# Kernel optimization log

Hardware: AMD Instinct MI355X
Metric: run time of the kernel (lower is better)

## Reference

```python
import jax, jax.numpy as jnp
import numpy as np

DIM = 1024

def _circ_conv(x, key):
    # circular convolution along last dim via FFT
    D = x.shape[-1]
    return jnp.fft.irfft(jnp.fft.rfft(x, axis=-1) * jnp.fft.rfft(key), n=D, axis=-1)

def _circ_corr(x, key):
    # circular correlation: conjugate the key spectrum
    D = x.shape[-1]
    return jnp.fft.irfft(jnp.fft.rfft(x, axis=-1) * jnp.conj(jnp.fft.rfft(key)), n=D, axis=-1)

def setup_inputs() -> dict:
    key = jax.random.key(0)
    k0, k1, k2 = jax.random.split(key, 3)
    B, T, D = 4, 2048, DIM
    x = jax.random.normal(k0, (B, T, D), dtype=jnp.float32)
    bind_key = jax.random.normal(k1, (D,), dtype=jnp.float32) * 0.02
    unbind_key = jax.random.normal(k2, (D,), dtype=jnp.float32) * 0.02
    gate = jnp.ones((1,), dtype=jnp.float32)
    decay = jnp.asarray(0.9, dtype=jnp.float32)
    return {"x": x, "bind_key": bind_key, "unbind_key": unbind_key, "gate": gate, "decay": decay}

def reference(x, bind_key, unbind_key, gate, decay):
    B, T, D = x.shape
    bound = _circ_conv(x, bind_key)                      # (B, T, D)
    d = jax.nn.sigmoid(decay)
    pos = jnp.arange(T, dtype=x.dtype)
    diff = pos[:, None] - pos[None, :]                   # (T, T)
    causal = diff >= 0
    # clamp exponent to avoid inf*0 on masked (t < s) entries; math identical to tril mask
    decay_matrix = jnp.where(causal, d ** jnp.maximum(diff, 0.0), 0.0)
    hologram = jnp.einsum('ts,bsd->btd', decay_matrix, bound)
    retrieved = _circ_corr(hologram, unbind_key)
    return x + gate * retrieved
```

## Files before the change

kernel.cpp:

```cpp
#include <hip/hip_runtime.h>
#include <hip/hip_bf16.h>

constexpr int Dd = 1024;
constexpr int Tt = 2048;
constexpr int Bb = 4;
constexpr int Rr = Bb * Tt;
constexpr int RSN = 1032;
constexpr int BM  = 128;
constexpr int BN  = 128;
constexpr int BK  = 64;
constexpr int NST = Dd / BK;

typedef __attribute__((ext_vector_type(2))) float f32x2;
typedef __attribute__((ext_vector_type(16))) float f32x16;
typedef __attribute__((ext_vector_type(8))) short bf16x8;

__device__ __forceinline__ float sigmoidf_(float v) {
    return 1.0f / (1.0f + expf(-v));
}

__global__ void k_c(const float* __restrict__ bind,
                    const float* __restrict__ unbind,
                    float* __restrict__ c) {
    __shared__ float sb[Dd];
    __shared__ float su[Dd];
    __shared__ float sp[256];
    const int tid = threadIdx.x;
    for (int j = tid; j < Dd; j += 256) { sb[j] = bind[j]; su[j] = unbind[j]; }
    __syncthreads();
    const int n_loc = tid >> 4;
    const int seg = tid & 15;
    const int n = (int)blockIdx.x * 16 + n_loc;
    float acc = 0.f;
    #pragma unroll 8
    for (int i = 0; i < 64; ++i) {
        const int m = i * 16 + seg;
        acc = fmaf(su[m], sb[(m + n) & (Dd - 1)], acc);
    }
    sp[tid] = acc;
    __syncthreads();
    if (tid < 16) {
        float s = 0.f;
        #pragma unroll
        for (int j = 0; j < 16; ++j) s += sp[tid * 16 + j];
        c[(int)blockIdx.x * 16 + tid] = s;
    }
}

__global__ __launch_bounds__(256, 2) void k_fused(
    const float* __restrict__ x,
    const float* __restrict__ c,
    const float* __restrict__ decay,
    const float* __restrict__ gate,
    float* __restrict__ out)
{
    __shared__ __align__(16) __hip_bfloat16 sA[2][BM * BK];
    __shared__ __align__(16) __hip_bfloat16 rs[8][RSN];
    __shared__ float cs[Dd];
    __shared__ float sS[10][BK];

    const int tid = threadIdx.x;
    const int wave = tid >> 6;
    const int lane = tid & 63;

    const int id  = blockIdx.x;
    const int xcd = id & 7;
    const int rr  = id >> 3;
    const int in_ = rr & 7;
    const int gg  = rr >> 3;
    const int im  = xcd * 8 + gg;
    const int tile_m = im * BM;
    const int tile_n = in_ * BN;
    const int pw  = im & 15;

    const float dd = sigmoidf_(decay[0]);
    const float d2 = dd * dd, d4 = d2 * d2, d8 = d4 * d4;
    const float d16 = d8 * d8, d32 = d16 * d16;

    #pragma unroll
    for (int j = 0; j < 4; ++j) cs[tid + j * 256] = c[tid + j * 256];
    __syncthreads();
    #pragma unroll
    for (int s = 0; s < 8; ++s)
        for (int t = tid; t < RSN; t += 256)
            rs[s][t] = __float2bfloat16(cs[(-(t + s)) & (Dd - 1)]);

    const int cp = tid & 31;
    const int s  = tid >> 5;
    const bool wdu  = (s >= 6);
    const bool wldz = (pw == 0);
    const int wrow  = tile_m - 32 + (s - 6) * 16;

    f32x2 vm[16];
    f32x2 vw[16];

    auto loadstrip = [&](int st) {
        const int col = st * BK + 2 * cp;
        const float* xp = x + (size_t)(tile_m + s * 16) * Dd + col;
        #pragma unroll
        for (int i = 0; i < 16; ++i)
            vm[i] = *(const f32x2*)&xp[(size_t)i * Dd];
        if (wdu && !wldz) {
            const float* wp = x + (size_t)wrow * Dd + col;
            #pragma unroll
            for (int i = 0; i < 16; ++i)
                vw[i] = *(const f32x2*)&wp[(size_t)i * Dd];
        }
    };

    auto chains = [&]() {
        #pragma unroll
        for (int i = 1; i < 16; ++i) vm[i] = dd * vm[i - 1] + vm[i];
        *(f32x2*)&sS[s][2 * cp] = vm[15];
        if (wdu) {
            f32x2 sw = (f32x2){0.f, 0.f};
            if (!wldz) {
                sw = vw[0];
                #pragma unroll
                for (int i = 1; i < 16; ++i) sw = dd * sw + vw[i];
            }
            *(f32x2*)&sS[8 + (s - 6)][2 * cp] = sw;
        }
    };

    auto loadS = [&](int r) -> f32x2 {
        if (r >= 0)  return *(const f32x2*)&sS[r][2 * cp];
        if (r == -1) return *(const f32x2*)&sS[9][2 * cp];
        if (r == -2) return *(const f32x2*)&sS[8][2 * cp];
        return (f32x2){0.f, 0.f};
    };

    auto finish = [&](int bb2) {
        f32x2 C = loadS(s - 1) + d16 * loadS(s - 2) + d32 * loadS(s - 3);
        float w = dd;
        #pragma unroll
        for (int i = 0; i < 16; ++i) {
            f32x2 h = vm[i] + w * C;
            w *= dd;
            const int rl = s * 16 + i;
            const int pos = (((2 * cp) >> 3) ^ (rl & 7)) * 8 + (2 * cp & 7);
            ushort2 o;
            union { __hip_bfloat16 b; unsigned short u; } ux, uy;
            ux.b = __float2bfloat16(h[0]);
            uy.b = __float2bfloat16(h[1]);
            o.x = ux.u; o.y = uy.u;
            *(ushort2*)&sA[bb2][rl * 64 + pos] = o;
        }
    };

    const int wm  = (wave & 1) * 64;
    const int wn  = (wave >> 1) * 64;
    const int fm  = lane & 31;
    const int fsw = fm & 7;
    const int fc0 = lane >> 5;
    const int ng0 = tile_n + wn + fm;

    f32x16 acc[2][2];
    #pragma unroll
    for (int i = 0; i < 2; ++i)
        #pragma unroll
        for (int j = 0; j < 2; ++j)
            #pragma unroll
            for (int e = 0; e < 16; ++e)
                acc[i][j][e] = 0.f;

    loadstrip(0);
    chains();
    __syncthreads();
    finish(0);
    __syncthreads();

    for (int st = 0; st < NST; ++st) {
        const int bb = st & 1;
        if (st + 1 < NST) loadstrip(st + 1);

        const int k0 = st * BK;
        #pragma unroll
        for (int kh = 0; kh < 4; ++kh) {
            const int kc = kh * 2 + fc0;
            const int ck = k0 + kc * 8;
            bf16x8 af[2], bfr[2];
            #pragma unroll
            for (int sm = 0; sm < 2; ++sm)
                af[sm] = *(const bf16x8*)
                    &sA[bb][(wm + sm * 32 + fm) * 64 + (kc ^ fsw) * 8];
            #pragma unroll
            for (int sn = 0; sn < 2; ++sn) {
                const int bi = (ck - (ng0 + sn * 32)) & (Dd - 1);
                bfr[sn] = *(const bf16x8*)&rs[bi & 7][bi & ~7];
            }
            #pragma unroll
            for (int sm = 0; sm < 2; ++sm)
                #pragma unroll
                for (int sn = 0; sn < 2; ++sn)
                    acc[sm][sn] = __builtin_amdgcn_mfma_f32_32x32x16_bf16(
                        af[sm], bfr[sn], acc[sm][sn], 0, 0, 0);
        }

        if (st + 1 < NST) {
            chains();
            __syncthreads();
            finish(bb ^ 1);
        }
        __syncthreads();
    }

    const float g = gate[0];
    #pragma unroll
    for (int sm = 0; sm < 2; ++sm) {
        #pragma unroll
        for (int sn = 0; sn < 2; ++sn) {
            const int colg = tile_n + wn + sn * 32 + (lane & 31);
            #pragma unroll
            for (int g1 = 0; g1 < 4; ++g1) {
                const int row0 = tile_m + wm + sm * 32 + g1 * 8 + (lane >> 5) * 4;
                #pragma unroll
                for (int r0 = 0; r0 < 4; ++r0) {
                    const size_t off = (size_t)(row0 + r0) * Dd + colg;
                    out[off] = fmaf(g, acc[sm][sn][g1 * 4 + r0], x[off]);
                }
            }
        }
    }
}

extern "C" void kernel_launch(void* const* d_in, const int* in_sizes, int n_in,
                              void* d_out, int out_size, void* d_ws, size_t ws_size,
                              hipStream_t stream) {
    const float* x      = (const float*)d_in[0];
    const float* bind   = (const float*)d_in[1];
    const float* unbind = (const float*)d_in[2];
    const float* gate   = (const float*)d_in[3];
    const float* decay  = (const float*)d_in[4];
    float* out = (float*)d_out;

    float* c = (float*)d_ws;

    k_c    <<<dim3(64),  dim3(256), 0, stream>>>(bind, unbind, c);
    k_fused<<<dim3(512), dim3(256), 0, stream>>>(x, c, decay, gate, out);
}
```

Before: 124.8 us.

## Precompute halo decay sums in prologue kernel and read key spectrum directly

```diff
diff --git a/kernel.cpp b/kernel.cpp
--- a/kernel.cpp
+++ b/kernel.cpp
@@ -21,42 +21,63 @@
 
 __global__ void k_c(const float* __restrict__ bind,
                     const float* __restrict__ unbind,
-                    float* __restrict__ c) {
-    __shared__ float sb[Dd];
-    __shared__ float su[Dd];
-    __shared__ float sp[256];
+                    const float* __restrict__ x,
+                    const float* __restrict__ decay,
+                    float* __restrict__ c,
+                    float* __restrict__ Sw) {
     const int tid = threadIdx.x;
-    for (int j = tid; j < Dd; j += 256) { sb[j] = bind[j]; su[j] = unbind[j]; }
-    __syncthreads();
-    const int n_loc = tid >> 4;
-    const int seg = tid & 15;
-    const int n = (int)blockIdx.x * 16 + n_loc;
-    float acc = 0.f;
-    #pragma unroll 8
-    for (int i = 0; i < 64; ++i) {
-        const int m = i * 16 + seg;
-        acc = fmaf(su[m], sb[(m + n) & (Dd - 1)], acc);
-    }
-    sp[tid] = acc;
-    __syncthreads();
-    if (tid < 16) {
-        float s = 0.f;
-        #pragma unroll
-        for (int j = 0; j < 16; ++j) s += sp[tid * 16 + j];
-        c[(int)blockIdx.x * 16 + tid] = s;
+    if (blockIdx.x < 64) {
+        __shared__ float sb[Dd];
+        __shared__ float su[Dd];
+        __shared__ float sp[256];
+        for (int j = tid; j < Dd; j += 256) { sb[j] = bind[j]; su[j] = unbind[j]; }
+        __syncthreads();
+        const int n_loc = tid >> 4;
+        const int seg = tid & 15;
+        const int n = (int)blockIdx.x * 16 + n_loc;
+        float acc = 0.f;
+        #pragma unroll 8
+        for (int i = 0; i < 64; ++i) {
+            const int m = i * 16 + seg;
+            acc = fmaf(su[m], sb[(m + n) & (Dd - 1)], acc);
+        }
+        sp[tid] = acc;
+        __syncthreads();
+        if (tid < 16) {
+            float s = 0.f;
+            #pragma unroll
+            for (int j = 0; j < 16; ++j) s += sp[tid * 16 + j];
+            c[(int)blockIdx.x * 16 + tid] = s;
+        }
+    } else {
+        const int w = (int)blockIdx.x - 64;
+        const int p = (w >> 1) + 1;
+        const int h = w & 1;
+        const float dd = sigmoidf_(decay[0]);
+        const int col = h * 512 + tid * 2;
+        const float* xp = x + (size_t)(p * BM - 32) * Dd + col;
+        f32x2 s8 = (f32x2){0.f, 0.f}, s9 = (f32x2){0.f, 0.f};
+        #pragma unroll
+        for (int i = 0; i < 16; ++i)
+            s8 = dd * s8 + *(const f32x2*)&xp[(size_t)i * Dd];
+        #pragma unroll
+        for (int i = 16; i < 32; ++i)
+            s9 = dd * s9 + *(const f32x2*)&xp[(size_t)i * Dd];
+        *(f32x2*)&Sw[((size_t)p * 2 + 0) * Dd + col] = s8;
+        *(f32x2*)&Sw[((size_t)p * 2 + 1) * Dd + col] = s9;
     }
 }
 
 __global__ __launch_bounds__(256, 2) void k_fused(
     const float* __restrict__ x,
     const float* __restrict__ c,
+    const float* __restrict__ Sw,
     const float* __restrict__ decay,
     const float* __restrict__ gate,
     float* __restrict__ out)
 {
     __shared__ __align__(16) __hip_bfloat16 sA[2][BM * BK];
     __shared__ __align__(16) __hip_bfloat16 rs[8][RSN];
-    __shared__ float cs[Dd];
     __shared__ float sS[10][BK];
 
     const int tid = threadIdx.x;
@@ -78,21 +99,16 @@
     const float d16 = d8 * d8, d32 = d16 * d16;
 
     #pragma unroll
-    for (int j = 0; j < 4; ++j) cs[tid + j * 256] = c[tid + j * 256];
-    __syncthreads();
-    #pragma unroll
     for (int s = 0; s < 8; ++s)
         for (int t = tid; t < RSN; t += 256)
-            rs[s][t] = __float2bfloat16(cs[(-(t + s)) & (Dd - 1)]);
+            rs[s][t] = __float2bfloat16(c[(-(t + s)) & (Dd - 1)]);
 
     const int cp = tid & 31;
     const int s  = tid >> 5;
-    const bool wdu  = (s >= 6);
     const bool wldz = (pw == 0);
-    const int wrow  = tile_m - 32 + (s - 6) * 16;
 
     f32x2 vm[16];
-    f32x2 vw[16];
+    f32x2 sw = (f32x2){0.f, 0.f};
 
     auto loadstrip = [&](int st) {
         const int col = st * BK + 2 * cp;
@@ -100,27 +116,17 @@
         #pragma unroll
         for (int i = 0; i < 16; ++i)
             vm[i] = *(const f32x2*)&xp[(size_t)i * Dd];
-        if (wdu && !wldz) {
-            const float* wp = x + (size_t)wrow * Dd + col;
-            #pragma unroll
-            for (int i = 0; i < 16; ++i)
-                vw[i] = *(const f32x2*)&wp[(size_t)i * Dd];
-        }
+        if (s >= 6 && !wldz)
+            sw = *(const f32x2*)&Sw[((size_t)im * 2 + (s - 6)) * Dd + col];
     };
 
     auto chains = [&]() {
         #pragma unroll
         for (int i = 1; i < 16; ++i) vm[i] = dd * vm[i - 1] + vm[i];
         *(f32x2*)&sS[s][2 * cp] = vm[15];
-        if (wdu) {
-            f32x2 sw = (f32x2){0.f, 0.f};
-            if (!wldz) {
-                sw = vw[0];
-                #pragma unroll
-                for (int i = 1; i < 16; ++i) sw = dd * sw + vw[i];
-            }
-            *(f32x2*)&sS[8 + (s - 6)][2 * cp] = sw;
-        }
+        if (s >= 6)
+            *(f32x2*)&sS[8 + (s - 6)][2 * cp] =
+                wldz ? (f32x2){0.f, 0.f} : sw;
     };
 
     auto loadS = [&](int r) -> f32x2 {
@@ -234,8 +240,9 @@
     const float* decay  = (const float*)d_in[4];
     float* out = (float*)d_out;
 
-    float* c = (float*)d_ws;
-
-    k_c    <<<dim3(64),  dim3(256), 0, stream>>>(bind, unbind, c);
-    k_fused<<<dim3(512), dim3(256), 0, stream>>>(x, c, decay, gate, out);
-}
+    float* c  = (float*)d_ws;
+    float* Sw = (float*)((char*)d_ws + 4096);
+
+    k_c    <<<dim3(190), dim3(256), 0, stream>>>(bind, unbind, x, decay, c, Sw);
+    k_fused<<<dim3(512), dim3(256), 0, stream>>>(x, c, Sw, decay, gate, out);
+}
```

Result: faster. 120.3 us, median of 2 (-3.6%).
